# Performance work log

Measured on AMD Instinct MI355X. Metric: run time of the kernel, lower is better.

The kernel has to match this reference:

```python
import jax, jax.numpy as jnp
import numpy as np

NUM_HEADS = 8
CHUNK = 64          # dialtion / chunck_size
EPS = 1e-5          # InstanceNorm1d eps
NEG = -1e9


def setup_inputs() -> dict:
    key = jax.random.key(0)
    ks = jax.random.split(key, 8)
    N, C, T = 4, 512, 4096
    x = jax.random.normal(ks[0], (N, C, T), dtype=jnp.float32)
    q = jax.random.normal(ks[1], (N, C, T), dtype=jnp.float32)
    k = jax.random.normal(ks[2], (N, C, T), dtype=jnp.float32)
    v = jax.random.normal(ks[3], (N, C, T), dtype=jnp.float32)
    masks = jnp.ones((N, 1, T), dtype=jnp.float32)
    s = 1.0 / np.sqrt(C)
    W_in = jax.random.normal(ks[4], (3 * C, C), dtype=jnp.float32) * s   # packed q/k/v in-proj
    b_in = jnp.zeros((3 * C,), dtype=jnp.float32)
    W_out = jax.random.normal(ks[5], (C, C), dtype=jnp.float32) * s     # out-proj
    b_out = jnp.zeros((C,), dtype=jnp.float32)
    return {"x": x, "q": q, "k": k, "v": v, "masks": masks,
            "W_in": W_in, "b_in": b_in, "W_out": W_out, "b_out": b_out}


def _chunk_attn(q, k, v, masks, W_in, b_in, W_out, b_out):
    # q,k,v: [N, C, T]; masks: [N, 1, T]
    N, C, T = q.shape
    H, Dh = NUM_HEADS, C // NUM_HEADS
    nc = T // CHUNK
    Wq, Wk, Wv = jnp.split(W_in, 3, axis=0)
    bq, bk, bv = jnp.split(b_in, 3, axis=0)

    def proj(t, W, b):
        # [N,C,T] -> chunked heads [N, nc, CHUNK, H, Dh]
        t = t.transpose(0, 2, 1) @ W.T + b            # [N, T, C]
        return t.reshape(N, nc, CHUNK, H, Dh)

    qh = proj(q, Wq, bq)
    kh = proj(k, Wk, bk)
    vh = proj(v, Wv, bv)

    scale = 1.0 / jnp.sqrt(jnp.asarray(Dh, q.dtype))
    # intra-chunk scores: [N, nc, H, CHUNK, CHUNK]
    scores = jnp.einsum('bnqhd,bnkhd->bnhqk', qh, kh) * scale
    km = masks[:, 0, :].reshape(N, nc, CHUNK)         # key validity per chunk
    scores = scores + jnp.where(km[:, :, None, None, :] > 0, 0.0, NEG)
    attn = jax.nn.softmax(scores, axis=-1)
    out = jnp.einsum('bnhqk,bnkhd->bnqhd', attn, vh).reshape(N, T, C)
    out = out @ W_out.T + b_out                        # [N, T, C]
    out = out.transpose(0, 2, 1) * masks               # [N, C, T], re-mask
    return out


def reference(x, q, k, v, masks, W_in, b_in, W_out, b_out):
    out = _chunk_attn(q, k, v, masks, W_in, b_in, W_out, b_out) + x
    # InstanceNorm1d (affine=False): normalize each (n, c) row over T
    mu = jnp.mean(out, axis=2, keepdims=True)
    var = jnp.mean(jnp.square(out - mu), axis=2, keepdims=True)
    return (out - mu) * jax.lax.rsqrt(var + EPS)
```

## Files before the change

kernel.cpp:

```cpp
#include <hip/hip_runtime.h>
#include <hip/hip_bf16.h>

#define NB 4
#define CC 512
#define TT 4096
#define C3 1536
#define CQK 1024
#define NTC (NB*TT*CC)

typedef __attribute__((ext_vector_type(4))) float f32x4;
typedef __attribute__((ext_vector_type(8))) short short8;
typedef unsigned short ushort;
typedef __attribute__((ext_vector_type(8))) ushort u16x8;

__device__ __forceinline__ ushort f2bf(float f){
    union { float f; unsigned u; } x; x.f = f;
    unsigned r = x.u + 0x7fffu + ((x.u >> 16) & 1u);
    return (ushort)(r >> 16);
}

__device__ __forceinline__ ushort2 pk2bf(float a, float b){
    float2 f2; f2.x = a; f2.y = b;
    __hip_bfloat162 h = __float22bfloat162_rn(f2);
    union { __hip_bfloat162 h2; ushort2 u2; } u; u.h2 = h;
    return u.u2;
}

__device__ __forceinline__ void gload16(const void* g, void* l){
    __builtin_amdgcn_global_load_lds((const __attribute__((address_space(1))) void*)g,
                                     (__attribute__((address_space(3))) void*)l,
                                     16, 0, 0);
}

__device__ __forceinline__ int apos(int m, int cb){
    return (m*8 + ((cb + m + (m >> 3)) & 7))*8;
}

__global__ __launch_bounds__(256) void wcvt(const float* __restrict__ Wi,
                                            const float* __restrict__ Wo,
                                            ushort* __restrict__ Wb,
                                            ushort* __restrict__ Wob){
    int idx0 = blockIdx.x * 1024 + threadIdx.x;
    for (int i = 0; i < 4; ++i){
        int idx = idx0 + i*256;
        const float* src; ushort* dst; int j;
        if (idx < 196608){ src = Wi; dst = Wb;  j = idx; }
        else             { src = Wo; dst = Wob; j = idx - 196608; }
        f32x4 vv = *((const f32x4*)src + j);
        ushort4 o;
        *(ushort2*)&o.x = pk2bf(vv[0], vv[1]);
        *(ushort2*)&o.z = pk2bf(vv[2], vv[3]);
        *((ushort4*)dst + j) = o;
    }
}

__global__ __launch_bounds__(256) void proj_gemm(const float* __restrict__ q,
                                                 const float* __restrict__ k,
                                                 const float* __restrict__ v,
                                                 const ushort* __restrict__ Wb,
                                                 const float* __restrict__ b_in,
                                                 ushort* __restrict__ P,
                                                 ushort* __restrict__ Vt){
    __shared__ __align__(16) ushort smem[128*136];
    ushort* sA = smem;
    ushort* sB = smem + 128*64;
    const int tid = threadIdx.x;
    const int bid = blockIdx.x;
    const int mtile  = ((bid & 7) << 4) | ((bid >> 3) & 15);
    const int cotile = bid >> 7;
    const int co0 = cotile * 128;
    const int m0  = mtile * 128;
    const int which = co0 >> 9;
    const float* src = (which == 0) ? q : (which == 1) ? k : v;
    const int n  = m0 >> 12, t0 = m0 & 4095;
    const ushort* Bbase = Wb + (size_t)co0*CC;
    const int w = tid >> 6, lane = tid & 63;
    const int wr = w >> 1, wc = w & 1;
    const int l15 = lane & 15, quad = lane >> 4;

    const int cbA = (w << 1) | (lane >> 5);
    const int tA  = lane & 31;
    const float* Abase = src + (size_t)n*CC*TT + (size_t)(cbA*8)*TT + t0 + tA*4;

    const ushort* gB[4]; ushort* lB[4];
    for (int i = 0; i < 4; ++i){
        int slot = i*256 + tid;
        int mr = slot >> 3, k8 = slot & 7, kk = k8 ^ (mr & 7);
        gB[i] = Bbase + (size_t)mr*CC + kk*8;
        lB[i] = sB + (i*256 + (tid & ~63)) * 8;
    }

    f32x4 acc[4][4] = {};
    f32x4 cur[8], nxt[8];
    #pragma unroll
    for (int j = 0; j < 8; ++j)
        cur[j] = *(const f32x4*)(Abase + (size_t)j*TT);

    for (int kb = 0; kb < 8; ++kb){
        __syncthreads();
        #pragma unroll
        for (int tj = 0; tj < 4; ++tj){
            int m = tA*4 + tj;
            u16x8 o;
            #pragma unroll
            for (int j = 0; j < 8; j += 2){
                ushort2 p = pk2bf(cur[j][tj], cur[j+1][tj]);
                o[j] = p.x; o[j+1] = p.y;
            }
            *(u16x8*)&sA[apos(m, cbA)] = o;
        }
        for (int i = 0; i < 4; ++i) gload16(gB[i] + kb*64, lB[i]);
        __syncthreads();
        if (kb < 7){
            const float* Ab = Abase + (size_t)((kb+1)*64)*TT;
            #pragma unroll
            for (int j = 0; j < 8; ++j)
                nxt[j] = *(const f32x4*)(Ab + (size_t)j*TT);
        }
        for (int ks = 0; ks < 2; ++ks){
            short8 aF[4], bF[4];
            for (int mi = 0; mi < 4; ++mi){
                int m = wr*64 + mi*16 + l15;
                aF[mi] = *(const short8*)&sA[apos(m, ks*4 + quad)];
            }
            for (int ni = 0; ni < 4; ++ni){
                int m = wc*64 + ni*16 + l15;
                bF[ni] = *(const short8*)&sB[(m*8 + ((ks*4 + quad) ^ (m & 7)))*8];
            }
            for (int mi = 0; mi < 4; ++mi)
                for (int ni = 0; ni < 4; ++ni)
                    acc[mi][ni] = __builtin_amdgcn_mfma_f32_16x16x32_bf16(
                        aF[mi], bF[ni], acc[mi][ni], 0, 0, 0);
        }
        if (kb < 7){
            #pragma unroll
            for (int j = 0; j < 8; ++j) cur[j] = nxt[j];
        }
    }

    float bj[4];
    for (int ni = 0; ni < 4; ++ni) bj[ni] = b_in[co0 + wc*64 + ni*16 + l15];

    __syncthreads();
    ushort* sOut = smem;
    if (which < 2){
        for (int mi = 0; mi < 4; ++mi){
            int mrow = wr*64 + mi*16 + quad*4;
            for (int ni = 0; ni < 4; ++ni){
                int col = wc*64 + ni*16 + l15;
                for (int r = 0; r < 4; ++r)
                    sOut[(mrow + r)*136 + col] = f2bf(acc[mi][ni][r] + bj[ni]);
            }
        }
    } else {
        for (int mi = 0; mi < 4; ++mi){
            int mrow = wr*64 + mi*16 + quad*4;
            for (int ni = 0; ni < 4; ++ni){
                int col = wc*64 + ni*16 + l15;
                ushort4 o4;
                o4.x = f2bf(acc[mi][ni][0] + bj[ni]);
                o4.y = f2bf(acc[mi][ni][1] + bj[ni]);
                o4.z = f2bf(acc[mi][ni][2] + bj[ni]);
                o4.w = f2bf(acc[mi][ni][3] + bj[ni]);
                *(ushort4*)&sOut[col*136 + mrow] = o4;
            }
        }
    }
    __syncthreads();
    if (which < 2){
        for (int i = 0; i < 8; ++i){
            int flat = i*256 + tid;
            int row = flat >> 4, cs = (flat & 15)*8;
            u16x8 val = *(const u16x8*)&sOut[row*136 + cs];
            *(u16x8*)(P + (size_t)(m0 + row)*CQK + which*512 + (co0 & 511) + cs) = val;
        }
    } else {
        for (int i = 0; i < 8; ++i){
            int flat = i*256 + tid;
            int row = flat >> 4, cs = (flat & 15)*8;
            int cl = (co0 - 1024) + row;
            int h = cl >> 6, d = cl & 63;
            u16x8 val = *(const u16x8*)&sOut[row*136 + cs];
            *(u16x8*)(Vt + (((size_t)n*8 + h)*64 + d)*TT + t0 + cs) = val;
        }
    }
}

__global__ __launch_bounds__(256) void attn_kernel(const ushort* __restrict__ P,
                                                   const ushort* __restrict__ Vt,
                                                   const float* __restrict__ masks,
                                                   ushort* __restrict__ ctx){
    __shared__ __align__(16) ushort sQ[64*64], sK[64*64], sV[64*64];
    __shared__ __align__(16) ushort sP[64][72];
    __shared__ __align__(16) ushort sO[64*72];
    int bid = blockIdx.x;
    int h = bid & 7, ch = (bid >> 3) & 63, n = bid >> 9;
    const int tid = threadIdx.x, lane = tid & 63, w = tid >> 6;
    const int l15 = lane & 15, quad = lane >> 4;
    const size_t rowbase = (size_t)n*TT + (size_t)ch*64;
    for (int i = 0; i < 2; ++i){
        int slot = i*256 + tid;
        int r = slot >> 3, k8 = slot & 7, kk = k8 ^ (r & 7);
        int lbase = (i*256 + (tid & ~63)) * 8;
        const ushort* gq = P + (rowbase + r)*CQK + h*64 + kk*8;
        gload16(gq,        sQ + lbase);
        gload16(gq + 512,  sK + lbase);
        const ushort* gv = Vt + (((size_t)n*8 + h)*64 + r)*TT + ch*64 + kk*8;
        gload16(gv,        sV + lbase);
    }
    __syncthreads();
    const int m0w = w*16;
    short8 aQ[2]; f32x4 accS[4] = {};
    for (int ks = 0; ks < 2; ++ks){
        int m = m0w + l15;
        aQ[ks] = *(const short8*)&sQ[(m*8 + ((ks*4 + quad) ^ (m & 7)))*8];
    }
    for (int ni = 0; ni < 4; ++ni)
        for (int ks = 0; ks < 2; ++ks){
            int m = ni*16 + l15;
            short8 bK = *(const short8*)&sK[(m*8 + ((ks*4 + quad) ^ (m & 7)))*8];
            accS[ni] = __builtin_amdgcn_mfma_f32_16x16x32_bf16(aQ[ks], bK, accS[ni], 0,0,0);
        }
    float madd[4];
    for (int ni = 0; ni < 4; ++ni){
        float mv = masks[(size_t)n*TT + ch*64 + ni*16 + l15];
        madd[ni] = (mv > 0.f) ? 0.f : -1e9f;
    }
    float s[4][4];
    for (int ni = 0; ni < 4; ++ni)
        for (int r = 0; r < 4; ++r) s[ni][r] = accS[ni][r]*0.125f + madd[ni];
    float ex[4][4];
    for (int r = 0; r < 4; ++r){
        float m1 = fmaxf(fmaxf(s[0][r], s[1][r]), fmaxf(s[2][r], s[3][r]));
        for (int d = 1; d < 16; d <<= 1) m1 = fmaxf(m1, __shfl_xor(m1, d));
        float a = 0.f;
        for (int ni = 0; ni < 4; ++ni){ float e = __expf(s[ni][r] - m1); ex[ni][r] = e; a += e; }
        for (int d = 1; d < 16; d <<= 1) a += __shfl_xor(a, d);
        float rs = 1.0f / a;
        for (int ni = 0; ni < 4; ++ni)
            sP[m0w + quad*4 + r][ni*16 + l15] = f2bf(ex[ni][r] * rs);
    }
    short8 aP[2]; f32x4 accO[4] = {};
    for (int ks = 0; ks < 2; ++ks)
        aP[ks] = *(const short8*)&sP[m0w + l15][ks*32 + quad*8];
    for (int ni = 0; ni < 4; ++ni)
        for (int ks = 0; ks < 2; ++ks){
            int m = ni*16 + l15;
            short8 bV = *(const short8*)&sV[(m*8 + ((ks*4 + quad) ^ (m & 7)))*8];
            accO[ni] = __builtin_amdgcn_mfma_f32_16x16x32_bf16(aP[ks], bV, accO[ni], 0,0,0);
        }
    for (int ni = 0; ni < 4; ++ni)
        for (int r = 0; r < 4; ++r)
            sO[(m0w + quad*4 + r)*72 + ni*16 + l15] = f2bf(accO[ni][r]);
    __syncthreads();
    for (int i = 0; i < 2; ++i){
        int flat = i*256 + tid;
        int row = flat >> 3, cs = (flat & 7)*8;
        u16x8 val = *(const u16x8*)&sO[row*72 + cs];
        *(u16x8*)(ctx + (rowbase + row)*CC + h*64 + cs) = val;
    }
}

__global__ __launch_bounds__(256) void out_gemm(const ushort* __restrict__ ctx,
                                                const ushort* __restrict__ Wob,
                                                const float* __restrict__ b_out,
                                                const float* __restrict__ x,
                                                const float* __restrict__ masks,
                                                float* __restrict__ out){
    __shared__ __align__(16) ushort smem[16896];
    ushort* sA = smem;
    ushort* sB = smem + 128*64;
    float* fOut = (float*)smem;
    const int tid = threadIdx.x;
    const int bid = blockIdx.x;
    const int mtile  = ((bid & 7) << 4) | ((bid >> 3) & 15);
    const int cotile = bid >> 7;
    const int co0 = cotile * 64;
    const int m0  = mtile * 128;
    const int n = m0 >> 12, t0 = m0 & 4095;
    const ushort* Abase = ctx + (size_t)m0*CC;
    const ushort* Bbase = Wob + (size_t)co0*CC;
    const int w = tid >> 6, lane = tid & 63;
    const int wr = w >> 1, wc = w & 1;
    const int l15 = lane & 15, quad = lane >> 4;

    const ushort* gA[4]; ushort* lA[4];
    const ushort* gB[2]; ushort* lB[2];
    for (int i = 0; i < 4; ++i){
        int slot = i*256 + tid;
        int m = slot >> 3, k8 = slot & 7, kk = k8 ^ (m & 7);
        gA[i] = Abase + (size_t)m*CC + kk*8;
        lA[i] = sA + (i*256 + (tid & ~63)) * 8;
    }
    for (int i = 0; i < 2; ++i){
        int slot = i*256 + tid;
        int m = slot >> 3, k8 = slot & 7, kk = k8 ^ (m & 7);
        gB[i] = Bbase + (size_t)m*CC + kk*8;
        lB[i] = sB + (i*256 + (tid & ~63)) * 8;
    }

    f32x4 acc[4][2] = {};
    for (int kb = 0; kb < 8; ++kb){
        __syncthreads();
        for (int i = 0; i < 4; ++i) gload16(gA[i] + kb*64, lA[i]);
        for (int i = 0; i < 2; ++i) gload16(gB[i] + kb*64, lB[i]);
        __syncthreads();
        for (int ks = 0; ks < 2; ++ks){
            short8 aF[4], bF[2];
            for (int mi = 0; mi < 4; ++mi){
                int m = wr*64 + mi*16 + l15;
                aF[mi] = *(const short8*)&sA[(m*8 + ((ks*4 + quad) ^ (m & 7)))*8];
            }
            for (int ni = 0; ni < 2; ++ni){
                int m = wc*32 + ni*16 + l15;
                bF[ni] = *(const short8*)&sB[(m*8 + ((ks*4 + quad) ^ (m & 7)))*8];
            }
            for (int mi = 0; mi < 4; ++mi)
                for (int ni = 0; ni < 2; ++ni)
                    acc[mi][ni] = __builtin_amdgcn_mfma_f32_16x16x32_bf16(
                        aF[mi], bF[ni], acc[mi][ni], 0, 0, 0);
        }
    }
    float bo[2];
    for (int ni = 0; ni < 2; ++ni) bo[ni] = b_out[co0 + wc*32 + ni*16 + l15];

    __syncthreads();
    for (int mi = 0; mi < 4; ++mi){
        int tl = wr*64 + mi*16 + quad*4;
        for (int ni = 0; ni < 2; ++ni){
            int cl = wc*32 + ni*16 + l15;
            f32x4 vv;
            for (int r = 0; r < 4; ++r) vv[r] = acc[mi][ni][r] + bo[ni];
            *(f32x4*)&fOut[cl*132 + tl] = vv;
        }
    }
    __syncthreads();
    for (int i = 0; i < 8; ++i){
        int flat = i*256 + tid;
        int co = flat >> 5, ts = (flat & 31)*4;
        f32x4 a = *(const f32x4*)&fOut[co*132 + ts];
        f32x4 mk = *(const f32x4*)(masks + (size_t)n*TT + t0 + ts);
        f32x4 xv = *(const f32x4*)(x + ((size_t)n*CC + co0 + co)*TT + t0 + ts);
        f32x4 o;
        for (int r = 0; r < 4; ++r) o[r] = a[r]*mk[r] + xv[r];
        *(f32x4*)(out + ((size_t)n*CC + co0 + co)*TT + t0 + ts) = o;
    }
}

__global__ __launch_bounds__(256) void inorm(float* __restrict__ out){
    __shared__ float sS[4], sQ2[4];
    float* row = out + (size_t)blockIdx.x * TT;
    f32x4 vbuf[4];
    float s = 0.f, ss = 0.f;
    for (int i = 0; i < 4; ++i){
        f32x4 vv = *(const f32x4*)(row + (size_t)(i*256 + threadIdx.x)*4);
        vbuf[i] = vv;
        for (int r = 0; r < 4; ++r){ s += vv[r]; ss += vv[r]*vv[r]; }
    }
    for (int d = 1; d < 64; d <<= 1){ s += __shfl_xor(s, d); ss += __shfl_xor(ss, d); }
    int w = threadIdx.x >> 6;
    if ((threadIdx.x & 63) == 0){ sS[w] = s; sQ2[w] = ss; }
    __syncthreads();
    s  = sS[0] + sS[1] + sS[2] + sS[3];
    ss = sQ2[0] + sQ2[1] + sQ2[2] + sQ2[3];
    float mean = s * (1.0f/TT);
    float var  = ss * (1.0f/TT) - mean*mean;
    float rstd = rsqrtf(var + 1e-5f);
    for (int i = 0; i < 4; ++i){
        f32x4 vv = vbuf[i], o;
        for (int r = 0; r < 4; ++r) o[r] = (vv[r] - mean) * rstd;
        *(f32x4*)(row + (size_t)(i*256 + threadIdx.x)*4) = o;
    }
}

extern "C" void kernel_launch(void* const* d_in, const int* in_sizes, int n_in,
                              void* d_out, int out_size, void* d_ws, size_t ws_size,
                              hipStream_t stream) {
    const float* x     = (const float*)d_in[0];
    const float* q     = (const float*)d_in[1];
    const float* k     = (const float*)d_in[2];
    const float* v     = (const float*)d_in[3];
    const float* masks = (const float*)d_in[4];
    const float* W_in  = (const float*)d_in[5];
    const float* b_in  = (const float*)d_in[6];
    const float* W_out = (const float*)d_in[7];
    const float* b_out = (const float*)d_in[8];
    float* out = (float*)d_out;

    ushort* ws  = (ushort*)d_ws;
    ushort* ctx = ws;
    ushort* Wb  = ws + (size_t)NTC;
    ushort* Wob = Wb + 786432;
    ushort* P   = Wob + 262144;
    ushort* Vt  = P + (size_t)NB*TT*CQK;

    wcvt<<<256, 256, 0, stream>>>(W_in, W_out, Wb, Wob);
    proj_gemm<<<1536, 256, 0, stream>>>(q, k, v, Wb, b_in, P, Vt);
    attn_kernel<<<2048, 256, 0, stream>>>(P, Vt, masks, ctx);
    out_gemm<<<1024, 256, 0, stream>>>(ctx, Wob, b_out, x, masks, out);
    inorm<<<2048, 256, 0, stream>>>(out);
}
```

Measured before the change: 244.4 us.

## Stage projection GEMM A and B tiles via async LDS loads with double-buffered B

The projection GEMM now brings the fp32 activation tile into a raw LDS staging buffer with direct global-to-LDS loads instead of through register prefetch, and double-buffers the bf16 weight tile so the next k-block's loads are issued before the current MFMA work. The aim is to overlap global memory latency with compute and to free the registers that held the prefetched activations. In exchange, LDS use grows to about 80KB per block, which may lower occupancy, and the loop relies on the barrier ordering to keep the raw buffer from being overwritten while still being read.

After: 239.9 us. Within noise of the previous version (-1.8%).

```diff
diff --git a/kernel.cpp b/kernel.cpp
--- a/kernel.cpp
+++ b/kernel.cpp
@@ -61,9 +61,11 @@
                                                  const float* __restrict__ b_in,
                                                  ushort* __restrict__ P,
                                                  ushort* __restrict__ Vt){
-    __shared__ __align__(16) ushort smem[128*136];
-    ushort* sA = smem;
-    ushort* sB = smem + 128*64;
+    __shared__ __align__(16) ushort smem[40960];
+    ushort* sA   = smem;
+    ushort* sB0  = smem + 8192;
+    ushort* sB1  = smem + 16384;
+    float*  Araw = (float*)(smem + 24576);
     const int tid = threadIdx.x;
     const int bid = blockIdx.x;
     const int mtile  = ((bid & 7) << 4) | ((bid >> 3) & 15);
@@ -78,26 +80,36 @@
     const int wr = w >> 1, wc = w & 1;
     const int l15 = lane & 15, quad = lane >> 4;
 
-    const int cbA = (w << 1) | (lane >> 5);
-    const int tA  = lane & 31;
-    const float* Abase = src + (size_t)n*CC*TT + (size_t)(cbA*8)*TT + t0 + tA*4;
-
-    const ushort* gB[4]; ushort* lB[4];
+    const int rowoff = lane >> 5;
+    const int toff   = (lane & 31) * 4;
+    const float* Ag = src + (size_t)n*CC*TT + (size_t)(2*w + rowoff)*TT + t0 + toff;
+    float* lAr = Araw + (size_t)(2*w)*128;
+
+    const ushort* gB[4]; int lBoff[4];
     for (int i = 0; i < 4; ++i){
         int slot = i*256 + tid;
         int mr = slot >> 3, k8 = slot & 7, kk = k8 ^ (mr & 7);
         gB[i] = Bbase + (size_t)mr*CC + kk*8;
-        lB[i] = sB + (i*256 + (tid & ~63)) * 8;
-    }
+        lBoff[i] = (i*256 + (tid & ~63)) * 8;
+    }
+
+    const int cbA = (w << 1) | (lane >> 5);
+    const int tA  = lane & 31;
+
+    for (int r = 0; r < 8; ++r)
+        gload16(Ag + (size_t)(r*8)*TT, lAr + r*1024);
+    for (int i = 0; i < 4; ++i)
+        gload16(gB[i], sB0 + lBoff[i]);
 
     f32x4 acc[4][4] = {};
-    f32x4 cur[8], nxt[8];
-    #pragma unroll
-    for (int j = 0; j < 8; ++j)
-        cur[j] = *(const f32x4*)(Abase + (size_t)j*TT);
-
     for (int kb = 0; kb < 8; ++kb){
+        ushort* sBc = (kb & 1) ? sB1 : sB0;
+        ushort* sBn = (kb & 1) ? sB0 : sB1;
         __syncthreads();
+        f32x4 cur[8];
+        #pragma unroll
+        for (int j = 0; j < 8; ++j)
+            cur[j] = *(const f32x4*)(Araw + (size_t)(cbA*8 + j)*128 + tA*4);
         #pragma unroll
         for (int tj = 0; tj < 4; ++tj){
             int m = tA*4 + tj;
@@ -109,13 +121,13 @@
             }
             *(u16x8*)&sA[apos(m, cbA)] = o;
         }
-        for (int i = 0; i < 4; ++i) gload16(gB[i] + kb*64, lB[i]);
         __syncthreads();
         if (kb < 7){
-            const float* Ab = Abase + (size_t)((kb+1)*64)*TT;
-            #pragma unroll
-            for (int j = 0; j < 8; ++j)
-                nxt[j] = *(const f32x4*)(Ab + (size_t)j*TT);
+            const float* Agn = Ag + (size_t)((kb+1)*64)*TT;
+            for (int r = 0; r < 8; ++r)
+                gload16(Agn + (size_t)(r*8)*TT, lAr + r*1024);
+            for (int i = 0; i < 4; ++i)
+                gload16(gB[i] + (kb+1)*64, sBn + lBoff[i]);
         }
         for (int ks = 0; ks < 2; ++ks){
             short8 aF[4], bF[4];
@@ -125,16 +137,12 @@
             }
             for (int ni = 0; ni < 4; ++ni){
                 int m = wc*64 + ni*16 + l15;
-                bF[ni] = *(const short8*)&sB[(m*8 + ((ks*4 + quad) ^ (m & 7)))*8];
+                bF[ni] = *(const short8*)&sBc[(m*8 + ((ks*4 + quad) ^ (m & 7)))*8];
             }
             for (int mi = 0; mi < 4; ++mi)
                 for (int ni = 0; ni < 4; ++ni)
                     acc[mi][ni] = __builtin_amdgcn_mfma_f32_16x16x32_bf16(
                         aF[mi], bF[ni], acc[mi][ni], 0, 0, 0);
-        }
-        if (kb < 7){
-            #pragma unroll
-            for (int j = 0; j < 8; ++j) cur[j] = nxt[j];
         }
     }
 
```
